# Kernel tuning notes

Measured on AMD Instinct MI355X. Metric: run time of the kernel, lower is better.

Reference implementation:

```python
import jax, jax.numpy as jnp
import numpy as np

N = 30000      # nodes
E = 480000     # edges (before self-loops)
IN = 32        # input_dim
H = 8          # heads
C = 64         # hidden_dim (per-head out channels)
HC = H * C     # 512, concat width
L = 3          # num_layers
NEG_SLOPE = 0.2  # PyG GATConv default


def setup_inputs() -> dict:
    key = jax.random.key(0)
    ks = jax.random.split(key, 16)
    s = 0.05
    return {
        "x": jax.random.normal(ks[0], (N, IN), jnp.float32),
        "edge_index": jax.random.randint(ks[1], (2, E), 0, N, jnp.int32),
        # input projection
        "W_in": jax.random.normal(ks[2], (IN, HC), jnp.float32) * s,
        "b_in": jnp.zeros((HC,), jnp.float32),
        # stacked GATConv params (L layers)
        "W_gat": jax.random.normal(ks[3], (L, HC, HC), jnp.float32) * s,
        "att_src": jax.random.normal(ks[4], (L, H, C), jnp.float32) * s,
        "att_dst": jax.random.normal(ks[5], (L, H, C), jnp.float32) * s,
        "b_gat": jnp.zeros((L, HC), jnp.float32),
        # heads
        "W_att": jax.random.normal(ks[6], (HC, H), jnp.float32) * s,
        "b_att": jnp.zeros((H,), jnp.float32),
        "W_h1": jax.random.normal(ks[7], (HC, C), jnp.float32) * s,
        "b_h1": jnp.zeros((C,), jnp.float32),
        "W_h2": jax.random.normal(ks[8], (C, 1), jnp.float32) * s,
        "b_h2": jnp.zeros((1,), jnp.float32),
    }


def _gat_layer(h, src, dst, W, a_src, a_dst, b):
    # h: [N, HC]; src/dst: [E'] (with self-loops)
    hp = (h @ W).reshape(N, H, C)                       # per-head features
    s = jnp.einsum('nhc,hc->nh', hp, a_src)             # [N, H]
    d = jnp.einsum('nhc,hc->nh', hp, a_dst)             # [N, H]
    e = jax.nn.leaky_relu(s[src] + d[dst], NEG_SLOPE)   # [E', H]
    # segment softmax over destination neighborhoods
    m = jax.ops.segment_max(e, dst, num_segments=N)     # [N, H]
    ex = jnp.exp(e - m[dst])
    den = jax.ops.segment_sum(ex, dst, num_segments=N)
    alpha = ex / (den[dst] + 1e-16)                     # [E', H]
    msg = hp[src] * alpha[:, :, None]                   # [E', H, C]
    out = jax.ops.segment_sum(msg, dst, num_segments=N).reshape(N, HC) + b
    return out


def reference(x, edge_index, W_in, b_in, W_gat, att_src, att_dst, b_gat,
              W_att, b_att, W_h1, b_h1, W_h2, b_h2):
    # PyG GATConv adds self-loops by default
    loops = jnp.arange(N, dtype=edge_index.dtype)
    src = jnp.concatenate([edge_index[0], loops])
    dst = jnp.concatenate([edge_index[1], loops])

    h = jax.nn.relu(x @ W_in + b_in)                    # input_proj + ReLU
    for l in range(L):
        h = jax.nn.relu(_gat_layer(h, src, dst, W_gat[l], att_src[l], att_dst[l], b_gat[l]))
        # dropout is identity in eval mode
    attention_weights = jax.nn.softmax(h @ W_att + b_att, axis=1)   # [N, H]
    anomaly_scores = jax.nn.sigmoid(jax.nn.relu(h @ W_h1 + b_h1) @ W_h2 + b_h2)  # [N, 1]
    return (anomaly_scores, attention_weights)
```

## Files before the change

### kernel.cpp

```cpp
#include <hip/hip_runtime.h>
#include <hip/hip_bf16.h>
#include <math.h>

#define HCW 512
#define NHD 8
#define CCH 64

typedef unsigned short u16;
typedef unsigned int   u32;
typedef __attribute__((ext_vector_type(8))) short bf16x8;
typedef __attribute__((ext_vector_type(4))) float f32x4;

__device__ __forceinline__ float bf2f(u32 u) {
  union { float f; u32 i; } v; v.i = u << 16; return v.f;
}
__device__ __forceinline__ u16 f2bf(float f) {
  u32 x = __builtin_bit_cast(u32, f);
  return (u16)((x + 0x7fff + ((x >> 16) & 1)) >> 16);
}
__device__ __forceinline__ void gload_lds16(const void* g, void* l) {
  __builtin_amdgcn_global_load_lds(
      (const __attribute__((address_space(1))) u32*)g,
      (__attribute__((address_space(3))) u32*)l, 16, 0, 0);
}

__global__ void k_hist(const int* __restrict__ ei, int* __restrict__ deg, int E, int N) {
  int e = blockIdx.x * blockDim.x + threadIdx.x;
  if (e >= E + N) return;
  int dst = (e < E) ? ei[E + e] : (e - E);
  atomicAdd(&deg[dst], 1);
}

__global__ __launch_bounds__(256) void k_scan1(const int* __restrict__ deg, int* __restrict__ ptr,
                                               int* __restrict__ bsum, int n) {
  __shared__ int sm[256];
  int b = blockIdx.x, i = b * 256 + threadIdx.x;
  int v = (i < n) ? deg[i] : 0;
  sm[threadIdx.x] = v;
  __syncthreads();
  for (int off = 1; off < 256; off <<= 1) {
    int t = (threadIdx.x >= off) ? sm[threadIdx.x - off] : 0;
    __syncthreads();
    sm[threadIdx.x] += t;
    __syncthreads();
  }
  if (i < n) ptr[i + 1] = sm[threadIdx.x];
  if (threadIdx.x == 255) bsum[b] = sm[255];
}

__global__ __launch_bounds__(256) void k_scan2(const int* __restrict__ bsum, int* __restrict__ boff, int nb) {
  __shared__ int sm[256];
  int v = (threadIdx.x < nb) ? bsum[threadIdx.x] : 0;
  sm[threadIdx.x] = v;
  __syncthreads();
  for (int off = 1; off < 256; off <<= 1) {
    int t = (threadIdx.x >= off) ? sm[threadIdx.x - off] : 0;
    __syncthreads();
    sm[threadIdx.x] += t;
    __syncthreads();
  }
  if (threadIdx.x < nb) boff[threadIdx.x] = sm[threadIdx.x] - v;
}

__global__ __launch_bounds__(256) void k_scan3(int* __restrict__ ptr, const int* __restrict__ boff, int n) {
  int i = blockIdx.x * 256 + threadIdx.x;
  if (i == 0) ptr[0] = 0;
  if (i < n) ptr[i + 1] += boff[blockIdx.x];
}

__global__ void k_fill(const int* __restrict__ ei, const int* __restrict__ ptr,
                       int* __restrict__ cnt, int* __restrict__ csr_src, int E, int N) {
  int e = blockIdx.x * blockDim.x + threadIdx.x;
  if (e >= E + N) return;
  int src, dst;
  if (e < E) { src = ei[e]; dst = ei[E + e]; } else { src = e - E; dst = e - E; }
  int pos = ptr[dst] + atomicAdd(&cnt[dst], 1);
  csr_src[pos] = src;
}

__global__ __launch_bounds__(256) void k_wconv(const float* __restrict__ W, u16* __restrict__ Wt) {
  __shared__ float sm[32][33];
  int l = blockIdx.z;
  int k0 = blockIdx.y * 32, n0 = blockIdx.x * 32;
  const float* Wl = W + (size_t)l * HCW * HCW;
  u16* Wtl = Wt + (size_t)l * HCW * HCW;
  int tx = threadIdx.x & 31, ty = threadIdx.x >> 5;
  #pragma unroll
  for (int r = 0; r < 32; r += 8)
    sm[ty + r][tx] = Wl[(size_t)(k0 + ty + r) * HCW + n0 + tx];
  __syncthreads();
  #pragma unroll
  for (int r = 0; r < 32; r += 8)
    Wtl[(size_t)(n0 + ty + r) * HCW + k0 + tx] = f2bf(sm[tx][ty + r]);
}

__global__ __launch_bounds__(256) void k_wfconv(const float* __restrict__ W_h1,
                                                const float* __restrict__ W_att,
                                                u16* __restrict__ Wf) {
  int n = blockIdx.x;
  for (int k = threadIdx.x; k < 512; k += 256) {
    float v = 0.f;
    if (n < 64) v = W_h1[(size_t)k * 64 + n];
    else if (n < 72) v = W_att[(size_t)k * 8 + (n - 64)];
    Wf[(size_t)n * 512 + k] = f2bf(v);
  }
}

__global__ __launch_bounds__(256) void k_xconv(const float* __restrict__ x, u16* __restrict__ xb, int total) {
  int i = (blockIdx.x * 256 + threadIdx.x) * 8;
  if (i >= total) return;
  float4 a = *(const float4*)(x + i);
  float4 b = *(const float4*)(x + i + 4);
  uint4 o;
  o.x = (u32)f2bf(a.x) | ((u32)f2bf(a.y) << 16);
  o.y = (u32)f2bf(a.z) | ((u32)f2bf(a.w) << 16);
  o.z = (u32)f2bf(b.x) | ((u32)f2bf(b.y) << 16);
  o.w = (u32)f2bf(b.z) | ((u32)f2bf(b.w) << 16);
  *(uint4*)(xb + i) = o;
}

__global__ __launch_bounds__(256) void k_winconv(const float* __restrict__ W, u16* __restrict__ Wt) {
  int idx = blockIdx.x * 256 + threadIdx.x;
  int n = idx >> 5, k = idx & 31;
  Wt[idx] = f2bf(W[(size_t)k * HCW + n]);
}

__global__ __launch_bounds__(256) void k_inproj3(const u16* __restrict__ xb, const u16* __restrict__ Wt,
                                                 const float* __restrict__ b, u16* __restrict__ h, int N) {
  __shared__ u16 As[128 * 32];
  __shared__ u16 Bs[128 * 32];
  int tid = threadIdx.x, lane = tid & 63, w = tid >> 6;
  int bm = blockIdx.y * 128, bn = blockIdx.x * 128;
  #pragma unroll
  for (int it = 0; it < 4; it++) {
    int g = it * 256 + tid;
    if (g < 512) {
      int row = g >> 2, gb = g & 3, gs = gb ^ (row & 3);
      int ar = bm + row; if (ar >= N) ar = N - 1;
      gload_lds16(xb + (size_t)ar * 32 + gs * 8, &As[g * 8]);
    } else {
      int gg = g - 512;
      int row = gg >> 2, gb = gg & 3, gs = gb ^ (row & 3);
      gload_lds16(Wt + (size_t)(bn + row) * 32 + gs * 8, &Bs[gg * 8]);
    }
  }
  __syncthreads();
  bf16x8 af[2];
  #pragma unroll
  for (int i = 0; i < 2; i++) {
    int rowA = w * 32 + i * 16 + (lane & 15);
    int gA = (lane >> 4) ^ (rowA & 3);
    af[i] = *(const bf16x8*)&As[rowA * 32 + gA * 8];
  }
  f32x4 acc[2][8] = {};
  #pragma unroll
  for (int j = 0; j < 8; j++) {
    int rowB = j * 16 + (lane & 15);
    int gB = (lane >> 4) ^ (rowB & 3);
    bf16x8 bfr = *(const bf16x8*)&Bs[rowB * 32 + gB * 8];
    #pragma unroll
    for (int i = 0; i < 2; i++)
      acc[i][j] = __builtin_amdgcn_mfma_f32_16x16x32_bf16(af[i], bfr, acc[i][j], 0, 0, 0);
  }
  #pragma unroll
  for (int j = 0; j < 8; j++) {
    int col = bn + j * 16 + (lane & 15);
    float bb = b[col];
    #pragma unroll
    for (int i = 0; i < 2; i++) {
      #pragma unroll
      for (int r = 0; r < 4; r++) {
        int n = bm + w * 32 + i * 16 + (lane >> 4) * 4 + r;
        if (n < N) h[(size_t)n * HCW + col] = f2bf(fmaxf(acc[i][j][r] + bb, 0.f));
      }
    }
  }
}

__global__ __launch_bounds__(256) void k_gemm_mfma(const u16* __restrict__ A,
                                                   const u16* __restrict__ Bt,
                                                   u16* __restrict__ C, int M) {
  __shared__ u16 As[128 * 64];
  __shared__ u16 Bs[128 * 64];
  int tid = threadIdx.x;
  int lane = tid & 63, w = tid >> 6;
  int wr = w >> 1, wc = w & 1;
  int bm = blockIdx.y * 128, bn = blockIdx.x * 128;
  f32x4 acc[4][4] = {};
  for (int k0 = 0; k0 < 512; k0 += 64) {
    __syncthreads();
    #pragma unroll
    for (int it = 0; it < 4; it++) {
      int g = it * 256 + tid;
      int row = g >> 3;
      int gb = g & 7;
      int gs = gb ^ (row & 7);
      int ar = bm + row; if (ar >= M) ar = M - 1;
      gload_lds16(A + (size_t)ar * HCW + k0 + gs * 8, &As[g * 8]);
      gload_lds16(Bt + (size_t)(bn + row) * HCW + k0 + gs * 8, &Bs[g * 8]);
    }
    __syncthreads();
    #pragma unroll
    for (int ks = 0; ks < 2; ks++) {
      bf16x8 af[4], bfr[4];
      #pragma unroll
      for (int f = 0; f < 4; f++) {
        int rowA = wr * 64 + f * 16 + (lane & 15);
        int gA = ((ks * 4 + (lane >> 4)) ^ (rowA & 7));
        af[f] = *(const bf16x8*)&As[rowA * 64 + gA * 8];
        int rowB = wc * 64 + f * 16 + (lane & 15);
        int gB = ((ks * 4 + (lane >> 4)) ^ (rowB & 7));
        bfr[f] = *(const bf16x8*)&Bs[rowB * 64 + gB * 8];
      }
      #pragma unroll
      for (int i = 0; i < 4; i++)
        #pragma unroll
        for (int j = 0; j < 4; j++)
          acc[i][j] = __builtin_amdgcn_mfma_f32_16x16x32_bf16(af[i], bfr[j], acc[i][j], 0, 0, 0);
    }
  }
  int gr_base = bm + wr * 64;
  int gc_base = bn + wc * 64;
  #pragma unroll
  for (int i = 0; i < 4; i++) {
    #pragma unroll
    for (int j = 0; j < 4; j++) {
      int col = gc_base + j * 16 + (lane & 15);
      #pragma unroll
      for (int r = 0; r < 4; r++) {
        int rowg = gr_base + i * 16 + (lane >> 4) * 4 + r;
        if (rowg < M) C[(size_t)rowg * HCW + col] = f2bf(acc[i][j][r]);
      }
    }
  }
}

__global__ __launch_bounds__(256) void k_sd(const u16* __restrict__ hp, const float* __restrict__ a_src,
                                            const float* __restrict__ a_dst, float* __restrict__ s,
                                            float* __restrict__ d, int N) {
  int wave = threadIdx.x >> 6, lane = threadIdx.x & 63;
  int n = blockIdx.x * 4 + wave;
  if (n >= N) return;
  int head = lane >> 3, c0 = lane & 7;
  const u16* row = hp + (size_t)n * HCW + head * 64 + c0 * 8;
  uint4 v = *(const uint4*)row;
  u32 vv[4] = {v.x, v.y, v.z, v.w};
  float ps = 0.f, pd = 0.f;
  const float* as = a_src + head * 64 + c0 * 8;
  const float* ad = a_dst + head * 64 + c0 * 8;
  #pragma unroll
  for (int j = 0; j < 4; j++) {
    float lo = bf2f(vv[j] & 0xffff), hi = bf2f(vv[j] >> 16);
    ps += lo * as[2 * j] + hi * as[2 * j + 1];
    pd += lo * ad[2 * j] + hi * ad[2 * j + 1];
  }
  ps += __shfl_xor(ps, 1); pd += __shfl_xor(pd, 1);
  ps += __shfl_xor(ps, 2); pd += __shfl_xor(pd, 2);
  ps += __shfl_xor(ps, 4); pd += __shfl_xor(pd, 4);
  if (c0 == 0) { s[(size_t)n * NHD + head] = ps; d[(size_t)n * NHD + head] = pd; }
}

__global__ __launch_bounds__(256) void k_agg3(const int* __restrict__ ptr, const int* __restrict__ csr_src,
                                              const u16* __restrict__ hp, const float* __restrict__ s,
                                              const float* __restrict__ d, const float* __restrict__ bias,
                                              u16* __restrict__ hout, int N) {
  int wv = threadIdx.x >> 6, lane = threadIdx.x & 63;
  int n = blockIdx.x * 4 + wv;
  if (n >= N) return;
  int hd = lane >> 3;
  int c = lane * 8;
  int beg = ptr[n], end = ptr[n + 1];
  float dn = d[(size_t)n * NHD + hd];
  float acc[8] = {0.f, 0.f, 0.f, 0.f, 0.f, 0.f, 0.f, 0.f};
  float den = 0.f;

  int i = beg;
  for (; i + 4 <= end; i += 4) {
    int s0 = csr_src[i], s1 = csr_src[i + 1], s2 = csr_src[i + 2], s3 = csr_src[i + 3];
    float e0 = s[(size_t)s0 * NHD + hd] + dn;
    float e1 = s[(size_t)s1 * NHD + hd] + dn;
    float e2 = s[(size_t)s2 * NHD + hd] + dn;
    float e3 = s[(size_t)s3 * NHD + hd] + dn;
    uint4 v0 = *(const uint4*)(hp + (size_t)s0 * HCW + c);
    uint4 v1 = *(const uint4*)(hp + (size_t)s1 * HCW + c);
    uint4 v2 = *(const uint4*)(hp + (size_t)s2 * HCW + c);
    uint4 v3 = *(const uint4*)(hp + (size_t)s3 * HCW + c);
    e0 = (e0 > 0.f) ? e0 : 0.2f * e0;
    e1 = (e1 > 0.f) ? e1 : 0.2f * e1;
    e2 = (e2 > 0.f) ? e2 : 0.2f * e2;
    e3 = (e3 > 0.f) ? e3 : 0.2f * e3;
    float x0 = __expf(e0), x1 = __expf(e1), x2 = __expf(e2), x3 = __expf(e3);
    den += (x0 + x1) + (x2 + x3);
    u32 w0[4] = {v0.x, v0.y, v0.z, v0.w};
    u32 w1[4] = {v1.x, v1.y, v1.z, v1.w};
    u32 w2[4] = {v2.x, v2.y, v2.z, v2.w};
    u32 w3[4] = {v3.x, v3.y, v3.z, v3.w};
    #pragma unroll
    for (int j = 0; j < 4; j++) {
      acc[2 * j]     += x0 * bf2f(w0[j] & 0xffff) + x1 * bf2f(w1[j] & 0xffff)
                      + x2 * bf2f(w2[j] & 0xffff) + x3 * bf2f(w3[j] & 0xffff);
      acc[2 * j + 1] += x0 * bf2f(w0[j] >> 16)    + x1 * bf2f(w1[j] >> 16)
                      + x2 * bf2f(w2[j] >> 16)    + x3 * bf2f(w3[j] >> 16);
    }
  }
  for (; i < end; i++) {
    int s0 = csr_src[i];
    float e0 = s[(size_t)s0 * NHD + hd] + dn;
    uint4 v0 = *(const uint4*)(hp + (size_t)s0 * HCW + c);
    e0 = (e0 > 0.f) ? e0 : 0.2f * e0;
    float x0 = __expf(e0);
    den += x0;
    u32 w0[4] = {v0.x, v0.y, v0.z, v0.w};
    #pragma unroll
    for (int j = 0; j < 4; j++) {
      acc[2 * j]     += x0 * bf2f(w0[j] & 0xffff);
      acc[2 * j + 1] += x0 * bf2f(w0[j] >> 16);
    }
  }

  float inv = 1.f / (den + 1e-16f);
  float4 bv0 = *(const float4*)(bias + c);
  float4 bv1 = *(const float4*)(bias + c + 4);
  float bb[8] = {bv0.x, bv0.y, bv0.z, bv0.w, bv1.x, bv1.y, bv1.z, bv1.w};
  u32 out[4];
  #pragma unroll
  for (int j = 0; j < 4; j++) {
    float o0 = fmaxf(acc[2 * j] * inv + bb[2 * j], 0.f);
    float o1 = fmaxf(acc[2 * j + 1] * inv + bb[2 * j + 1], 0.f);
    out[j] = (u32)f2bf(o0) | ((u32)f2bf(o1) << 16);
  }
  *(uint4*)(hout + (size_t)n * HCW + c) = make_uint4(out[0], out[1], out[2], out[3]);
}

__global__ __launch_bounds__(256) void k_final2(const u16* __restrict__ A,
                                                const u16* __restrict__ Wf,
                                                const float* __restrict__ b_att,
                                                const float* __restrict__ b_h1,
                                                const float* __restrict__ W_h2,
                                                const float* __restrict__ b_h2,
                                                float* __restrict__ anomaly, float* __restrict__ attw,
                                                int M) {
  __shared__ u16 As[128 * 64];
  __shared__ u16 Bs[80 * 64];
  __shared__ float so[4][32][84];
  int tid = threadIdx.x;
  int lane = tid & 63, w = tid >> 6;
  int bm = blockIdx.x * 128;
  f32x4 acc[2][5] = {};
  for (int k0 = 0; k0 < 512; k0 += 64) {
    __syncthreads();
    #pragma unroll
    for (int it = 0; it < 7; it++) {
      int g = it * 256 + tid;
      if (g < 1024) {
        int row = g >> 3, gb = g & 7;
        int gs = gb ^ (row & 7);
        int ar = bm + row; if (ar >= M) ar = M - 1;
        gload_lds16(A + (size_t)ar * HCW + k0 + gs * 8, &As[g * 8]);
      } else if (g < 1664) {
        int gg = g - 1024;
        int row = gg >> 3, gb = gg & 7;
        int gs = gb ^ (row & 7);
        gload_lds16(Wf + (size_t)row * 512 + k0 + gs * 8, &Bs[gg * 8]);
      }
    }
    __syncthreads();
    #pragma unroll
    for (int ks = 0; ks < 2; ks++) {
      bf16x8 af[2], bfr[5];
      #pragma unroll
      for (int i = 0; i < 2; i++) {
        int rowA = w * 32 + i * 16 + (lane & 15);
        int gA = ((ks * 4 + (lane >> 4)) ^ (rowA & 7));
        af[i] = *(const bf16x8*)&As[rowA * 64 + gA * 8];
      }
      #pragma unroll
      for (int j = 0; j < 5; j++) {
        int rowB = j * 16 + (lane & 15);
        int gB = ((ks * 4 + (lane >> 4)) ^ (rowB & 7));
        bfr[j] = *(const bf16x8*)&Bs[rowB * 64 + gB * 8];
      }
      #pragma unroll
      for (int i = 0; i < 2; i++)
        #pragma unroll
        for (int j = 0; j < 5; j++)
          acc[i][j] = __builtin_amdgcn_mfma_f32_16x16x32_bf16(af[i], bfr[j], acc[i][j], 0, 0, 0);
    }
  }
  #pragma unroll
  for (int i = 0; i < 2; i++) {
    #pragma unroll
    for (int j = 0; j < 5; j++) {
      int col = j * 16 + (lane & 15);
      #pragma unroll
      for (int r = 0; r < 4; r++) {
        int row_l = i * 16 + (lane >> 4) * 4 + r;
        so[w][row_l][col] = acc[i][j][r];
      }
    }
  }
  int row_l = lane >> 1, half = lane & 1;
  int n = bm + w * 32 + row_l;
  if (n < M) {
    float hacc = 0.f;
    #pragma unroll
    for (int kk = 0; kk < 32; kk++) {
      int cc = half * 32 + kk;
      float v = fmaxf(so[w][row_l][cc] + b_h1[cc], 0.f);
      hacc += v * W_h2[cc];
    }
    hacc += __shfl_xor(hacc, 1);
    if (half == 0) {
      anomaly[n] = 1.f / (1.f + __expf(-(hacc + b_h2[0])));
    } else {
      float lg[8];
      float mx = -1e30f;
      #pragma unroll
      for (int j = 0; j < 8; j++) {
        lg[j] = so[w][row_l][64 + j] + b_att[j];
        mx = fmaxf(mx, lg[j]);
      }
      float sum = 0.f;
      #pragma unroll
      for (int j = 0; j < 8; j++) { lg[j] = __expf(lg[j] - mx); sum += lg[j]; }
      float inv = 1.f / sum;
      #pragma unroll
      for (int j = 0; j < 8; j++) attw[(size_t)n * 8 + j] = lg[j] * inv;
    }
  }
}

extern "C" void kernel_launch(void* const* d_in, const int* in_sizes, int n_in,
                              void* d_out, int out_size, void* d_ws, size_t ws_size,
                              hipStream_t stream) {
  const float* x       = (const float*)d_in[0];
  const int*   ei      = (const int*)d_in[1];
  const float* W_in    = (const float*)d_in[2];
  const float* b_in    = (const float*)d_in[3];
  const float* W_gat   = (const float*)d_in[4];
  const float* att_src = (const float*)d_in[5];
  const float* att_dst = (const float*)d_in[6];
  const float* b_gat   = (const float*)d_in[7];
  const float* W_att   = (const float*)d_in[8];
  const float* b_att   = (const float*)d_in[9];
  const float* W_h1    = (const float*)d_in[10];
  const float* b_h1    = (const float*)d_in[11];
  const float* W_h2    = (const float*)d_in[12];
  const float* b_h2    = (const float*)d_in[13];

  const int N  = in_sizes[0] / 32;
  const int E  = in_sizes[1] / 2;
  const int ET = E + N;

  char* ws = (char*)d_ws;
  size_t off = 0;
  auto alloc = [&](size_t bytes) -> void* {
    void* p = ws + off;
    off = (off + bytes + 255) & ~(size_t)255;
    return p;
  };
  u16* h     = (u16*)alloc((size_t)N * HCW * 2);
  u16* hp    = (u16*)alloc((size_t)N * HCW * 2);
  u16* Wt    = (u16*)alloc((size_t)3 * HCW * HCW * 2);
  u16* Wf    = (u16*)alloc((size_t)80 * 512 * 2);
  u16* xb    = (u16*)alloc((size_t)N * 32 * 2);
  u16* Wtin  = (u16*)alloc((size_t)512 * 32 * 2);
  float* sarr = (float*)alloc((size_t)N * NHD * 4);
  float* darr = (float*)alloc((size_t)N * NHD * 4);
  int* deg    = (int*)alloc((size_t)N * 4);
  int* ptr    = (int*)alloc((size_t)(N + 1) * 4);
  int* cnt    = (int*)alloc((size_t)N * 4);
  int* csr    = (int*)alloc((size_t)ET * 4);
  int* bsum   = (int*)alloc((size_t)1024 * 4);
  int* boff   = (int*)alloc((size_t)1024 * 4);

  float* anomaly = (float*)d_out;
  float* attw    = (float*)d_out + N;

  hipMemsetAsync(deg, 0, (size_t)N * 4, stream);
  hipMemsetAsync(cnt, 0, (size_t)N * 4, stream);

  int gbE = (ET + 255) / 256;
  int nb  = (N + 255) / 256;
  k_hist<<<gbE, 256, 0, stream>>>(ei, deg, E, N);
  k_scan1<<<nb, 256, 0, stream>>>(deg, ptr, bsum, N);
  k_scan2<<<1, 256, 0, stream>>>(bsum, boff, nb);
  k_scan3<<<nb, 256, 0, stream>>>(ptr, boff, N);
  k_fill<<<gbE, 256, 0, stream>>>(ei, ptr, cnt, csr, E, N);

  k_wconv<<<dim3(16, 16, 3), 256, 0, stream>>>(W_gat, Wt);
  k_wfconv<<<80, 256, 0, stream>>>(W_h1, W_att, Wf);
  k_xconv<<<(N * 32 / 8 + 255) / 256, 256, 0, stream>>>(x, xb, N * 32);
  k_winconv<<<64, 256, 0, stream>>>(W_in, Wtin);
  k_inproj3<<<dim3(4, (N + 127) / 128), 256, 0, stream>>>(xb, Wtin, b_in, h, N);

  dim3 ggrid(HCW / 128, (N + 127) / 128);
  for (int l = 0; l < 3; l++) {
    k_gemm_mfma<<<ggrid, 256, 0, stream>>>(h, Wt + (size_t)l * HCW * HCW, hp, N);
    k_sd<<<(N + 3) / 4, 256, 0, stream>>>(hp, att_src + (size_t)l * NHD * CCH,
                                          att_dst + (size_t)l * NHD * CCH, sarr, darr, N);
    k_agg3<<<(N + 3) / 4, 256, 0, stream>>>(ptr, csr, hp, sarr, darr,
                                            b_gat + (size_t)l * HCW, h, N);
  }

  k_final2<<<(N + 127) / 128, 256, 0, stream>>>(h, Wf, b_att, b_h1, W_h2, b_h2,
                                                anomaly, attw, N);
}
```

Baseline: 437.0 us.

## Fuse attention scores into GEMM epilogue and precompute bf16 softmax weights per edge

Computes the per-node source and destination attention scores inside the MFMA GEMM epilogue from the fp32 accumulators, which removes the separate k_sd pass that re-read hp. Adds a k_alpha kernel that computes normalised softmax weights per edge and head and stores them as bf16. The aggregation kernel then only gathers alpha and hp rows, unrolled 8 deep for more loads in flight. This adds an extra kernel and an alpha buffer of E'×8 bf16 per layer, and rounding alpha to bf16 adds some precision loss.

New measurement: 483.2 us. +10.6%, slower.

```diff
diff --git a/kernel.cpp b/kernel.cpp
--- a/kernel.cpp
+++ b/kernel.cpp
@@ -179,7 +179,12 @@
 
 __global__ __launch_bounds__(256) void k_gemm_mfma(const u16* __restrict__ A,
                                                    const u16* __restrict__ Bt,
-                                                   u16* __restrict__ C, int M) {
+                                                   u16* __restrict__ C,
+                                                   const float* __restrict__ a_src,
+                                                   const float* __restrict__ a_dst,
+                                                   float* __restrict__ sarr,
+                                                   float* __restrict__ darr,
+                                                   int M) {
   __shared__ u16 As[128 * 64];
   __shared__ u16 Bs[128 * 64];
   int tid = threadIdx.x;
@@ -233,36 +238,65 @@
       }
     }
   }
-}
-
-__global__ __launch_bounds__(256) void k_sd(const u16* __restrict__ hp, const float* __restrict__ a_src,
-                                            const float* __restrict__ a_dst, float* __restrict__ s,
-                                            float* __restrict__ d, int N) {
-  int wave = threadIdx.x >> 6, lane = threadIdx.x & 63;
-  int n = blockIdx.x * 4 + wave;
+  int head = (bn >> 6) + wc;
+  float asv[4], adv[4];
+  #pragma unroll
+  for (int j = 0; j < 4; j++) {
+    asv[j] = a_src[head * 64 + j * 16 + (lane & 15)];
+    adv[j] = a_dst[head * 64 + j * 16 + (lane & 15)];
+  }
+  #pragma unroll
+  for (int i = 0; i < 4; i++) {
+    #pragma unroll
+    for (int r = 0; r < 4; r++) {
+      float sv = acc[i][0][r] * asv[0] + acc[i][1][r] * asv[1]
+               + acc[i][2][r] * asv[2] + acc[i][3][r] * asv[3];
+      float dv = acc[i][0][r] * adv[0] + acc[i][1][r] * adv[1]
+               + acc[i][2][r] * adv[2] + acc[i][3][r] * adv[3];
+      sv += __shfl_xor(sv, 1); dv += __shfl_xor(dv, 1);
+      sv += __shfl_xor(sv, 2); dv += __shfl_xor(dv, 2);
+      sv += __shfl_xor(sv, 4); dv += __shfl_xor(dv, 4);
+      sv += __shfl_xor(sv, 8); dv += __shfl_xor(dv, 8);
+      if ((lane & 15) == 0) {
+        int rowg = gr_base + i * 16 + (lane >> 4) * 4 + r;
+        if (rowg < M) {
+          sarr[(size_t)rowg * NHD + head] = sv;
+          darr[(size_t)rowg * NHD + head] = dv;
+        }
+      }
+    }
+  }
+}
+
+__global__ __launch_bounds__(256) void k_alpha(const int* __restrict__ ptr, const int* __restrict__ csr_src,
+                                               const float* __restrict__ s, const float* __restrict__ d,
+                                               u16* __restrict__ alpha, int N) {
+  int wv = threadIdx.x >> 6, lane = threadIdx.x & 63;
+  int n = blockIdx.x * 4 + wv;
   if (n >= N) return;
-  int head = lane >> 3, c0 = lane & 7;
-  const u16* row = hp + (size_t)n * HCW + head * 64 + c0 * 8;
-  uint4 v = *(const uint4*)row;
-  u32 vv[4] = {v.x, v.y, v.z, v.w};
-  float ps = 0.f, pd = 0.f;
-  const float* as = a_src + head * 64 + c0 * 8;
-  const float* ad = a_dst + head * 64 + c0 * 8;
-  #pragma unroll
-  for (int j = 0; j < 4; j++) {
-    float lo = bf2f(vv[j] & 0xffff), hi = bf2f(vv[j] >> 16);
-    ps += lo * as[2 * j] + hi * as[2 * j + 1];
-    pd += lo * ad[2 * j] + hi * ad[2 * j + 1];
-  }
-  ps += __shfl_xor(ps, 1); pd += __shfl_xor(pd, 1);
-  ps += __shfl_xor(ps, 2); pd += __shfl_xor(pd, 2);
-  ps += __shfl_xor(ps, 4); pd += __shfl_xor(pd, 4);
-  if (c0 == 0) { s[(size_t)n * NHD + head] = ps; d[(size_t)n * NHD + head] = pd; }
-}
-
-__global__ __launch_bounds__(256) void k_agg3(const int* __restrict__ ptr, const int* __restrict__ csr_src,
-                                              const u16* __restrict__ hp, const float* __restrict__ s,
-                                              const float* __restrict__ d, const float* __restrict__ bias,
+  int hd = lane & 7, g = lane >> 3;
+  int beg = ptr[n], end = ptr[n + 1];
+  float dn = d[(size_t)n * NHD + hd];
+  float den = 0.f;
+  for (int i = beg + g; i < end; i += 8) {
+    float e = s[(size_t)csr_src[i] * NHD + hd] + dn;
+    e = (e > 0.f) ? e : 0.2f * e;
+    den += __expf(e);
+  }
+  den += __shfl_xor(den, 8);
+  den += __shfl_xor(den, 16);
+  den += __shfl_xor(den, 32);
+  float inv = 1.f / (den + 1e-16f);
+  for (int i = beg + g; i < end; i += 8) {
+    float e = s[(size_t)csr_src[i] * NHD + hd] + dn;
+    e = (e > 0.f) ? e : 0.2f * e;
+    alpha[(size_t)i * NHD + hd] = f2bf(__expf(e) * inv);
+  }
+}
+
+__global__ __launch_bounds__(256) void k_agg4(const int* __restrict__ ptr, const int* __restrict__ csr_src,
+                                              const u16* __restrict__ hp, const u16* __restrict__ alpha,
+                                              const float* __restrict__ bias,
                                               u16* __restrict__ hout, int N) {
   int wv = threadIdx.x >> 6, lane = threadIdx.x & 63;
   int n = blockIdx.x * 4 + wv;
@@ -270,63 +304,49 @@
   int hd = lane >> 3;
   int c = lane * 8;
   int beg = ptr[n], end = ptr[n + 1];
-  float dn = d[(size_t)n * NHD + hd];
   float acc[8] = {0.f, 0.f, 0.f, 0.f, 0.f, 0.f, 0.f, 0.f};
-  float den = 0.f;
 
   int i = beg;
-  for (; i + 4 <= end; i += 4) {
-    int s0 = csr_src[i], s1 = csr_src[i + 1], s2 = csr_src[i + 2], s3 = csr_src[i + 3];
-    float e0 = s[(size_t)s0 * NHD + hd] + dn;
-    float e1 = s[(size_t)s1 * NHD + hd] + dn;
-    float e2 = s[(size_t)s2 * NHD + hd] + dn;
-    float e3 = s[(size_t)s3 * NHD + hd] + dn;
-    uint4 v0 = *(const uint4*)(hp + (size_t)s0 * HCW + c);
-    uint4 v1 = *(const uint4*)(hp + (size_t)s1 * HCW + c);
-    uint4 v2 = *(const uint4*)(hp + (size_t)s2 * HCW + c);
-    uint4 v3 = *(const uint4*)(hp + (size_t)s3 * HCW + c);
-    e0 = (e0 > 0.f) ? e0 : 0.2f * e0;
-    e1 = (e1 > 0.f) ? e1 : 0.2f * e1;
-    e2 = (e2 > 0.f) ? e2 : 0.2f * e2;
-    e3 = (e3 > 0.f) ? e3 : 0.2f * e3;
-    float x0 = __expf(e0), x1 = __expf(e1), x2 = __expf(e2), x3 = __expf(e3);
-    den += (x0 + x1) + (x2 + x3);
-    u32 w0[4] = {v0.x, v0.y, v0.z, v0.w};
-    u32 w1[4] = {v1.x, v1.y, v1.z, v1.w};
-    u32 w2[4] = {v2.x, v2.y, v2.z, v2.w};
-    u32 w3[4] = {v3.x, v3.y, v3.z, v3.w};
-    #pragma unroll
-    for (int j = 0; j < 4; j++) {
-      acc[2 * j]     += x0 * bf2f(w0[j] & 0xffff) + x1 * bf2f(w1[j] & 0xffff)
-                      + x2 * bf2f(w2[j] & 0xffff) + x3 * bf2f(w3[j] & 0xffff);
-      acc[2 * j + 1] += x0 * bf2f(w0[j] >> 16)    + x1 * bf2f(w1[j] >> 16)
-                      + x2 * bf2f(w2[j] >> 16)    + x3 * bf2f(w3[j] >> 16);
+  for (; i + 8 <= end; i += 8) {
+    int sidx[8];
+    u32 aw[8];
+    uint4 v[8];
+    #pragma unroll
+    for (int u = 0; u < 8; u++) sidx[u] = csr_src[i + u];
+    #pragma unroll
+    for (int u = 0; u < 8; u++) aw[u] = alpha[(size_t)(i + u) * NHD + hd];
+    #pragma unroll
+    for (int u = 0; u < 8; u++) v[u] = *(const uint4*)(hp + (size_t)sidx[u] * HCW + c);
+    #pragma unroll
+    for (int u = 0; u < 8; u++) {
+      float a = bf2f(aw[u]);
+      u32 w0 = v[u].x, w1 = v[u].y, w2 = v[u].z, w3 = v[u].w;
+      acc[0] += a * bf2f(w0 & 0xffff); acc[1] += a * bf2f(w0 >> 16);
+      acc[2] += a * bf2f(w1 & 0xffff); acc[3] += a * bf2f(w1 >> 16);
+      acc[4] += a * bf2f(w2 & 0xffff); acc[5] += a * bf2f(w2 >> 16);
+      acc[6] += a * bf2f(w3 & 0xffff); acc[7] += a * bf2f(w3 >> 16);
     }
   }
   for (; i < end; i++) {
     int s0 = csr_src[i];
-    float e0 = s[(size_t)s0 * NHD + hd] + dn;
+    u32 aw = alpha[(size_t)i * NHD + hd];
     uint4 v0 = *(const uint4*)(hp + (size_t)s0 * HCW + c);
-    e0 = (e0 > 0.f) ? e0 : 0.2f * e0;
-    float x0 = __expf(e0);
-    den += x0;
-    u32 w0[4] = {v0.x, v0.y, v0.z, v0.w};
-    #pragma unroll
-    for (int j = 0; j < 4; j++) {
-      acc[2 * j]     += x0 * bf2f(w0[j] & 0xffff);
-      acc[2 * j + 1] += x0 * bf2f(w0[j] >> 16);
-    }
-  }
-
-  float inv = 1.f / (den + 1e-16f);
+    float a = bf2f(aw);
+    u32 w0 = v0.x, w1 = v0.y, w2 = v0.z, w3 = v0.w;
+    acc[0] += a * bf2f(w0 & 0xffff); acc[1] += a * bf2f(w0 >> 16);
+    acc[2] += a * bf2f(w1 & 0xffff); acc[3] += a * bf2f(w1 >> 16);
+    acc[4] += a * bf2f(w2 & 0xffff); acc[5] += a * bf2f(w2 >> 16);
+    acc[6] += a * bf2f(w3 & 0xffff); acc[7] += a * bf2f(w3 >> 16);
+  }
+
   float4 bv0 = *(const float4*)(bias + c);
   float4 bv1 = *(const float4*)(bias + c + 4);
   float bb[8] = {bv0.x, bv0.y, bv0.z, bv0.w, bv1.x, bv1.y, bv1.z, bv1.w};
   u32 out[4];
   #pragma unroll
   for (int j = 0; j < 4; j++) {
-    float o0 = fmaxf(acc[2 * j] * inv + bb[2 * j], 0.f);
-    float o1 = fmaxf(acc[2 * j + 1] * inv + bb[2 * j + 1], 0.f);
+    float o0 = fmaxf(acc[2 * j] + bb[2 * j], 0.f);
+    float o1 = fmaxf(acc[2 * j + 1] + bb[2 * j + 1], 0.f);
     out[j] = (u32)f2bf(o0) | ((u32)f2bf(o1) << 16);
   }
   *(uint4*)(hout + (size_t)n * HCW + c) = make_uint4(out[0], out[1], out[2], out[3]);
@@ -465,6 +485,7 @@
   u16* Wf    = (u16*)alloc((size_t)80 * 512 * 2);
   u16* xb    = (u16*)alloc((size_t)N * 32 * 2);
   u16* Wtin  = (u16*)alloc((size_t)512 * 32 * 2);
+  u16* alpha = (u16*)alloc((size_t)ET * NHD * 2);
   float* sarr = (float*)alloc((size_t)N * NHD * 4);
   float* darr = (float*)alloc((size_t)N * NHD * 4);
   int* deg    = (int*)alloc((size_t)N * 4);
@@ -496,10 +517,12 @@
 
   dim3 ggrid(HCW / 128, (N + 127) / 128);
   for (int l = 0; l < 3; l++) {
-    k_gemm_mfma<<<ggrid, 256, 0, stream>>>(h, Wt + (size_t)l * HCW * HCW, hp, N);
-    k_sd<<<(N + 3) / 4, 256, 0, stream>>>(hp, att_src + (size_t)l * NHD * CCH,
-                                          att_dst + (size_t)l * NHD * CCH, sarr, darr, N);
-    k_agg3<<<(N + 3) / 4, 256, 0, stream>>>(ptr, csr, hp, sarr, darr,
+    k_gemm_mfma<<<ggrid, 256, 0, stream>>>(h, Wt + (size_t)l * HCW * HCW, hp,
+                                           att_src + (size_t)l * NHD * CCH,
+                                           att_dst + (size_t)l * NHD * CCH,
+                                           sarr, darr, N);
+    k_alpha<<<(N + 3) / 4, 256, 0, stream>>>(ptr, csr, sarr, darr, alpha, N);
+    k_agg4<<<(N + 3) / 4, 256, 0, stream>>>(ptr, csr, hp, alpha,
                                             b_gat + (size_t)l * HCW, h, N);
   }
 
```

## Fuse attention score dot products into GEMM epilogue and remap blocks per XCD

Applied to the files above, without the earlier changes.

Computes the per-node, per-head source and destination attention logits directly from the fp32 MFMA accumulators in the GEMM epilogue, using lane shuffles to reduce across columns, and removes the separate k_sd kernel. Each GEMM wave covers one 64-wide head slice, so a single reduction per row produces one head value. The block index is also remapped so that consecutive row panels are spread across the 8 XCDs while each XCD's four column tiles of a panel stay together, aiming for better L2 reuse of A. The logits now come from unrounded fp32 values rather than the bf16-stored hp, and the grid is padded, so some blocks exit early.

Measured after the change: 429.3 us. No clear change (-1.8%).

```diff
diff --git a/kernel.cpp b/kernel.cpp
--- a/kernel.cpp
+++ b/kernel.cpp
@@ -179,13 +179,27 @@
 
 __global__ __launch_bounds__(256) void k_gemm_mfma(const u16* __restrict__ A,
                                                    const u16* __restrict__ Bt,
-                                                   u16* __restrict__ C, int M) {
+                                                   u16* __restrict__ C,
+                                                   const float* __restrict__ a_src,
+                                                   const float* __restrict__ a_dst,
+                                                   float* __restrict__ sarr,
+                                                   float* __restrict__ darr,
+                                                   int M) {
+  int nPanels = (M + 127) >> 7;
+  int lin = blockIdx.y * 4 + blockIdx.x;
+  int xcd = lin & 7;
+  int t = lin >> 3;
+  int bn_i = t & 3;
+  int p = t >> 2;
+  int bm_i = p * 8 + xcd;
+  if (bm_i >= nPanels) return;
+  int bm = bm_i * 128, bn = bn_i * 128;
+
   __shared__ u16 As[128 * 64];
   __shared__ u16 Bs[128 * 64];
   int tid = threadIdx.x;
   int lane = tid & 63, w = tid >> 6;
   int wr = w >> 1, wc = w & 1;
-  int bm = blockIdx.y * 128, bn = blockIdx.x * 128;
   f32x4 acc[4][4] = {};
   for (int k0 = 0; k0 < 512; k0 += 64) {
     __syncthreads();
@@ -233,34 +247,37 @@
       }
     }
   }
-}
-
-__global__ __launch_bounds__(256) void k_sd(const u16* __restrict__ hp, const float* __restrict__ a_src,
-                                            const float* __restrict__ a_dst, float* __restrict__ s,
-                                            float* __restrict__ d, int N) {
-  int wave = threadIdx.x >> 6, lane = threadIdx.x & 63;
-  int n = blockIdx.x * 4 + wave;
-  if (n >= N) return;
-  int head = lane >> 3, c0 = lane & 7;
-  const u16* row = hp + (size_t)n * HCW + head * 64 + c0 * 8;
-  uint4 v = *(const uint4*)row;
-  u32 vv[4] = {v.x, v.y, v.z, v.w};
-  float ps = 0.f, pd = 0.f;
-  const float* as = a_src + head * 64 + c0 * 8;
-  const float* ad = a_dst + head * 64 + c0 * 8;
+  int head = (bn >> 6) + wc;
+  float asv[4], adv[4];
   #pragma unroll
   for (int j = 0; j < 4; j++) {
-    float lo = bf2f(vv[j] & 0xffff), hi = bf2f(vv[j] >> 16);
-    ps += lo * as[2 * j] + hi * as[2 * j + 1];
-    pd += lo * ad[2 * j] + hi * ad[2 * j + 1];
-  }
-  ps += __shfl_xor(ps, 1); pd += __shfl_xor(pd, 1);
-  ps += __shfl_xor(ps, 2); pd += __shfl_xor(pd, 2);
-  ps += __shfl_xor(ps, 4); pd += __shfl_xor(pd, 4);
-  if (c0 == 0) { s[(size_t)n * NHD + head] = ps; d[(size_t)n * NHD + head] = pd; }
-}
-
-__global__ __launch_bounds__(256) void k_agg3(const int* __restrict__ ptr, const int* __restrict__ csr_src,
+    asv[j] = a_src[head * 64 + j * 16 + (lane & 15)];
+    adv[j] = a_dst[head * 64 + j * 16 + (lane & 15)];
+  }
+  #pragma unroll
+  for (int i = 0; i < 4; i++) {
+    #pragma unroll
+    for (int r = 0; r < 4; r++) {
+      float sv = acc[i][0][r] * asv[0] + acc[i][1][r] * asv[1]
+               + acc[i][2][r] * asv[2] + acc[i][3][r] * asv[3];
+      float dv = acc[i][0][r] * adv[0] + acc[i][1][r] * adv[1]
+               + acc[i][2][r] * adv[2] + acc[i][3][r] * adv[3];
+      sv += __shfl_xor(sv, 1); dv += __shfl_xor(dv, 1);
+      sv += __shfl_xor(sv, 2); dv += __shfl_xor(dv, 2);
+      sv += __shfl_xor(sv, 4); dv += __shfl_xor(dv, 4);
+      sv += __shfl_xor(sv, 8); dv += __shfl_xor(dv, 8);
+      if ((lane & 15) == 0) {
+        int rowg = gr_base + i * 16 + (lane >> 4) * 4 + r;
+        if (rowg < M) {
+          sarr[(size_t)rowg * NHD + head] = sv;
+          darr[(size_t)rowg * NHD + head] = dv;
+        }
+      }
+    }
+  }
+}
+
+__global__ __launch_bounds__(256) void k_agg6(const int* __restrict__ ptr, const int* __restrict__ csr_src,
                                               const u16* __restrict__ hp, const float* __restrict__ s,
                                               const float* __restrict__ d, const float* __restrict__ bias,
                                               u16* __restrict__ hout, int N) {
@@ -494,12 +511,15 @@
   k_winconv<<<64, 256, 0, stream>>>(W_in, Wtin);
   k_inproj3<<<dim3(4, (N + 127) / 128), 256, 0, stream>>>(xb, Wtin, b_in, h, N);
 
-  dim3 ggrid(HCW / 128, (N + 127) / 128);
+  int nPanels = (N + 127) / 128;
+  int nPanelsPad = ((nPanels + 7) / 8) * 8;
+  dim3 ggrid(4, nPanelsPad);
   for (int l = 0; l < 3; l++) {
-    k_gemm_mfma<<<ggrid, 256, 0, stream>>>(h, Wt + (size_t)l * HCW * HCW, hp, N);
-    k_sd<<<(N + 3) / 4, 256, 0, stream>>>(hp, att_src + (size_t)l * NHD * CCH,
-                                          att_dst + (size_t)l * NHD * CCH, sarr, darr, N);
-    k_agg3<<<(N + 3) / 4, 256, 0, stream>>>(ptr, csr, hp, sarr, darr,
+    k_gemm_mfma<<<ggrid, 256, 0, stream>>>(h, Wt + (size_t)l * HCW * HCW, hp,
+                                           att_src + (size_t)l * NHD * CCH,
+                                           att_dst + (size_t)l * NHD * CCH,
+                                           sarr, darr, N);
+    k_agg6<<<(N + 3) / 4, 256, 0, stream>>>(ptr, csr, hp, sarr, darr,
                                             b_gat + (size_t)l * HCW, h, N);
   }
 
```
